# Kernel tuning notes

Hardware: AMD Instinct MI355X
Metric: run time of the kernel (lower is better)

## Reference

```python
import jax, jax.numpy as jnp
from jax import lax
import numpy as np

B, DIM, H, W = 1, 1024, 24, 24
HEADS, GROUPS = 8, 4
TOPK_FRAC = 0.8
EPS = 1e-12


def setup_inputs() -> dict:
    key = jax.random.key(0)
    ks = jax.random.split(key, 5)
    t = GROUPS
    x = jax.random.normal(ks[0], (B, DIM, H, W), dtype=jnp.float32)
    # Conv3d(t, 3t, 1x1x1, bias=False): weight [3t, t]
    w_qkv = jax.random.normal(ks[1], (3 * t, t), dtype=jnp.float32) * 0.3
    # depthwise Conv3d(3t, 3t, (1,3,3), groups=3t): weight [3t, 3, 3]
    w_dw = jax.random.normal(ks[2], (3 * t, 3, 3), dtype=jnp.float32) * 0.2
    # temperature [1, heads, 1, 1]
    temperature = jnp.ones((1, HEADS, 1, 1), dtype=jnp.float32)
    # project_out Conv2d(dim, dim, 1): weight [dim, dim]
    w_proj = jax.random.normal(ks[3], (DIM, DIM), dtype=jnp.float32) * 0.02
    return {"x": x, "temperature": temperature, "w_qkv": w_qkv, "w_dw": w_dw, "w_proj": w_proj}


def _to_heads(u, b, t, cs, h, w):
    # [b, t, cs, h, w] -> [b, heads, ch, (h w t)]  (t fastest in flattened axis)
    ch = cs // HEADS
    u = u.reshape(b, t, HEADS, ch, h, w)
    u = u.transpose(0, 2, 3, 4, 5, 1)  # b, head, ch, h, w, t
    return u.reshape(b, HEADS, ch, h * w * t)


def reference(x, temperature, w_qkv, w_dw, w_proj):
    b, c, h, w = x.shape
    t = GROUPS
    cs = c // t
    xg = x.reshape(b, t, cs, h, w)
    # pointwise conv3d across group dim: [b, 3t, cs, h, w]
    qkv = jnp.einsum("btchw,st->bschw", xg, w_qkv)
    # depthwise (1,3,3) conv: fold cs into batch, 2D depthwise over (h, w)
    y = qkv.transpose(0, 2, 1, 3, 4).reshape(b * cs, 3 * t, h, w)
    kern = w_dw[:, None, :, :]  # [3t, 1, 3, 3]
    y = lax.conv_general_dilated(
        y, kern, window_strides=(1, 1), padding="SAME",
        dimension_numbers=("NCHW", "OIHW", "NCHW"), feature_group_count=3 * t)
    qkv = y.reshape(b, cs, 3 * t, h, w).transpose(0, 2, 1, 3, 4)
    q, k, v = qkv[:, :t], qkv[:, t:2 * t], qkv[:, 2 * t:]
    q = _to_heads(q, b, t, cs, h, w)
    k = _to_heads(k, b, t, cs, h, w)
    v = _to_heads(v, b, t, cs, h, w)
    # L2-normalize over token axis (dim=-1), torch eps semantics
    q = q / jnp.maximum(jnp.linalg.norm(q, axis=-1, keepdims=True), EPS)
    k = k / jnp.maximum(jnp.linalg.norm(k, axis=-1, keepdims=True), EPS)
    N = q.shape[-1]
    K = int(N * TOPK_FRAC)
    attn = jnp.einsum("bhcn,bhcm->bhnm", q, k) * temperature  # [b, heads, N, N]
    vals, idx = lax.top_k(attn, K)
    # scatter top-k values into a -inf matrix == where(mask>0, attn, -inf)
    bi = jnp.arange(b)[:, None, None, None]
    hi = jnp.arange(HEADS)[None, :, None, None]
    ni = jnp.arange(N)[None, None, :, None]
    masked = jnp.full_like(attn, -jnp.inf).at[bi, hi, ni, idx].set(vals)
    p = jax.nn.softmax(masked, axis=-1)
    out = jnp.einsum("bhnm,bhcm->bhcn", p, v)  # [b, heads, ch, N]
    ch = cs // HEADS
    out = out.reshape(b, HEADS, ch, h, w, t).transpose(0, 5, 1, 2, 3, 4).reshape(b, c, h, w)
    out = jnp.einsum("bchw,oc->bohw", out, w_proj)
    return x + out
```

## Files before the change

### kernel.cpp

```cpp
#include <hip/hip_runtime.h>
#include <math.h>

typedef unsigned int u32;
typedef unsigned long long u64;
typedef unsigned short u16;
typedef __attribute__((ext_vector_type(8))) short bf16x8;
typedef __attribute__((ext_vector_type(4))) float f32x4;

#define NHEADS 8
#define HH 24
#define WW 24
#define HW 576
#define CS 256
#define CHD 32
#define NN 2304
#define NGROUPS 4
#define TOPK 1843
#define DIM 1024
#define EPSN 1e-12f

__device__ __forceinline__ u32 fkey(float f) {
    u32 u = __float_as_uint(f);
    return u ^ ((u >> 31) ? 0xFFFFFFFFu : 0x80000000u);
}
__device__ __forceinline__ float fkey_inv(u32 k) {
    return __uint_as_float((k & 0x80000000u) ? (k ^ 0x80000000u) : ~k);
}
__device__ __forceinline__ u16 f2bf(float f) {
    u32 u = __float_as_uint(f);
    return (u16)((u + 0x7FFFu + ((u >> 16) & 1u)) >> 16);
}
__device__ __forceinline__ u32 shiftOf(u32 rg) {
    return (rg > 255u) ? (u32)(24 - __clz(rg)) : 0u;
}

__global__ __launch_bounds__(256) void qkv_conv_kernel(
    const float* __restrict__ x, const float* __restrict__ w_qkv,
    const float* __restrict__ w_dw,
    float* __restrict__ qb, float* __restrict__ kb, u16* __restrict__ vb16)
{
    __shared__ float xp[NGROUPS][26][26];
    __shared__ float wq[48];
    __shared__ float wd[108];
    int c = blockIdx.x;
    int tid = threadIdx.x;

    for (int i = tid; i < NGROUPS * 26 * 26; i += 256) ((float*)xp)[i] = 0.f;
    if (tid < 48) wq[tid] = w_qkv[tid];
    if (tid < 108) wd[tid] = w_dw[tid];
    __syncthreads();
    for (int i = tid; i < NGROUPS * HW; i += 256) {
        int t = i / HW, p = i % HW;
        int hh = p / WW, ww = p % WW;
        xp[t][hh + 1][ww + 1] = x[(size_t)(t * CS + c) * HW + p];
    }
    __syncthreads();

    int hd = c >> 5, ch = c & 31;
    for (int p = tid; p < HW; p += 256) {
        int hh = p / WW, ww = p % WW;
        float res[12];
        #pragma unroll
        for (int s = 0; s < 12; ++s) {
            float acc = 0.f;
            #pragma unroll
            for (int t = 0; t < NGROUPS; ++t) {
                float cv = 0.f;
                #pragma unroll
                for (int dh = 0; dh < 3; ++dh)
                    #pragma unroll
                    for (int dw = 0; dw < 3; ++dw)
                        cv += xp[t][hh + dh][ww + dw] * wd[s * 9 + dh * 3 + dw];
                acc += wq[s * 4 + t] * cv;
            }
            res[s] = acc;
        }
        #pragma unroll
        for (int tt = 0; tt < 4; ++tt) {
            int n = p * 4 + tt;
            size_t off = ((size_t)hd * CHD + ch) * NN + n;
            qb[off] = res[tt];
            kb[off] = res[4 + tt];
            vb16[off] = f2bf(res[8 + tt]);
        }
    }
}

__global__ __launch_bounds__(256) void norm_scale_kernel(
    const float* __restrict__ qb, const float* __restrict__ kb,
    float* __restrict__ scales)
{
    __shared__ float redf[5];
    int b = blockIdx.x;
    const float* rowp = ((b < 256) ? qb : kb) + (size_t)(b & 255) * NN;
    int tid = threadIdx.x;
    float ss = 0.f;
    for (int i = tid; i < NN; i += 256) { float v = rowp[i]; ss += v * v; }
    for (int off = 32; off > 0; off >>= 1) ss += __shfl_down(ss, off);
    int wid = tid >> 6, lane = tid & 63;
    if (lane == 0) redf[wid] = ss;
    __syncthreads();
    if (tid == 0)
        scales[b] = 1.f / fmaxf(sqrtf(redf[0] + redf[1] + redf[2] + redf[3]), EPSN);
}

__global__ __launch_bounds__(256) void transpose_cast_kernel(
    const float* __restrict__ qb, const float* __restrict__ kb,
    const float* __restrict__ scales,
    u16* __restrict__ Qt, u16* __restrict__ Kt)
{
    __shared__ float tile[32][33];
    int ntile = blockIdx.x;
    int h = blockIdx.y;
    int which = blockIdx.z;
    const float* src = which ? kb : qb;
    const float* scl = scales + which * 256;
    u16* dst = which ? Kt : Qt;
    int tid = threadIdx.x;
    int n0 = ntile * 32;
    #pragma unroll
    for (int cc = 0; cc < 32; cc += 8) {
        int c = cc + (tid >> 5);
        tile[c][tid & 31] = src[(size_t)(h * CHD + c) * NN + n0 + (tid & 31)]
                            * scl[h * CHD + c];
    }
    __syncthreads();
    int cgrp = tid & 7, nrow = tid >> 3;
    #pragma unroll
    for (int c0 = 0; c0 < 32; c0 += 16) {
        int c = c0 + cgrp * 2;
        u16 v0 = f2bf(tile[c][nrow]);
        u16 v1 = f2bf(tile[c + 1][nrow]);
        ushort2 v; v.x = v0; v.y = v1;
        *(ushort2*)(dst + ((size_t)h * NN + n0 + nrow) * CHD + c) = v;
    }
}

__global__ __launch_bounds__(256) void cast_wproj_kernel(
    const float* __restrict__ wp, u16* __restrict__ wpb)
{
    int i = blockIdx.x * 256 + threadIdx.x;
    float4 v = ((const float4*)wp)[i];
    ushort4 o;
    o.x = f2bf(v.x); o.y = f2bf(v.y); o.z = f2bf(v.z); o.w = f2bf(v.w);
    ((ushort4*)wpb)[i] = o;
}

__global__ __launch_bounds__(512, 2) void attn_fused3_kernel(
    const u16* __restrict__ Qt, const u16* __restrict__ Kt,
    const u16* __restrict__ Vb, const float* __restrict__ temp,
    u16* __restrict__ aoutT)
{
    __shared__ u32 hist[16][257];
    __shared__ u32 candK[16][64];
    __shared__ u32 candM[16][64];
    __shared__ u16 Pst[8][16][40];
    __shared__ u32 kminA[16], maxkA[16], shA[16], kloA[16], khiA[16],
                   remKA[16], stateA[16], TkeyA[16], candCnt[16];
    __shared__ int cutA[16];
    __shared__ float denomF[16];
    __shared__ u32 flagS;

    int tid = threadIdx.x;
    int lane = tid & 63;
    int w = tid >> 6;
    int q = lane >> 4;
    int cI = lane & 15;
    int h = blockIdx.x / 144;
    int n0 = (blockIdx.x % 144) * 16;

    for (int i = tid; i < 16 * 257; i += 512) ((u32*)hist)[i] = 0u;
    if (tid < 16) {
        kminA[tid] = 0xFFFFFFFFu; maxkA[tid] = 0u; candCnt[tid] = 0u;
        denomF[tid] = 0.f; stateA[tid] = 0u; cutA[tid] = NN - 1;
        remKA[tid] = TOPK; TkeyA[tid] = 0u;
    }
    __syncthreads();

    const u16* Qth = Qt + (size_t)h * NN * CHD;
    const u16* Kth = Kt + (size_t)h * NN * CHD;
    const u16* Vbh = Vb + (size_t)h * CHD * NN;
    float ts = temp[h];

    bf16x8 afrag = *(const bf16x8*)(Qth + (size_t)(n0 + cI) * CHD + q * 8);
    int mW = w * 288;
    const f32x4 zz = {0.f, 0.f, 0.f, 0.f};

    {
        u32 lmin[4], lmax[4];
        #pragma unroll
        for (int r = 0; r < 4; ++r) { lmin[r] = 0xFFFFFFFFu; lmax[r] = 0u; }
        #pragma unroll 2
        for (int t = 0; t < 18; ++t) {
            bf16x8 bfrag = *(const bf16x8*)(Kth + (size_t)(mW + t * 16 + cI) * CHD + q * 8);
            f32x4 a = __builtin_amdgcn_mfma_f32_16x16x32_bf16(afrag, bfrag, zz, 0, 0, 0);
            #pragma unroll
            for (int r = 0; r < 4; ++r) {
                u32 k = fkey(a[r] * ts);
                lmin[r] = min(lmin[r], k); lmax[r] = max(lmax[r], k);
            }
        }
        #pragma unroll
        for (int r = 0; r < 4; ++r) {
            #pragma unroll
            for (int mk = 1; mk < 16; mk <<= 1) {
                lmin[r] = min(lmin[r], (u32)__shfl_xor((int)lmin[r], mk));
                lmax[r] = max(lmax[r], (u32)__shfl_xor((int)lmax[r], mk));
            }
            if (cI == 0) {
                atomicMin(&kminA[4 * q + r], lmin[r]);
                atomicMax(&maxkA[4 * q + r], lmax[r]);
            }
        }
    }
    __syncthreads();
    if (tid < 16) shA[tid] = shiftOf(maxkA[tid] - kminA[tid]);
    __syncthreads();

    {
        u32 km[4], sh[4];
        #pragma unroll
        for (int r = 0; r < 4; ++r) { km[r] = kminA[4 * q + r]; sh[r] = shA[4 * q + r]; }
        #pragma unroll 2
        for (int t = 0; t < 18; ++t) {
            bf16x8 bfrag = *(const bf16x8*)(Kth + (size_t)(mW + t * 16 + cI) * CHD + q * 8);
            f32x4 a = __builtin_amdgcn_mfma_f32_16x16x32_bf16(afrag, bfrag, zz, 0, 0, 0);
            #pragma unroll
            for (int r = 0; r < 4; ++r) {
                u32 k = fkey(a[r] * ts);
                atomicAdd(&hist[4 * q + r][(k - km[r]) >> sh[r]], 1u);
            }
        }
    }
    __syncthreads();

    #pragma unroll
    for (int rr = 0; rr < 2; ++rr) {
        int r = 2 * w + rr;
        u32 c0 = hist[r][lane * 4 + 0];
        u32 c1 = hist[r][lane * 4 + 1];
        u32 c2 = hist[r][lane * 4 + 2];
        u32 c3 = hist[r][lane * 4 + 3];
        u32 s3 = c3, s2 = c2 + s3, s1 = c1 + s2, s0 = c0 + s1;
        u32 suf = s0;
        #pragma unroll
        for (int off = 1; off < 64; off <<= 1) {
            u32 t2 = (u32)__shfl_down((int)suf, off);
            if (lane + off < 64) suf += t2;
        }
        u32 above_lane = suf - s0;
        u32 sArr[4] = {s0, s1, s2, s3};
        u32 cArr[4] = {c0, c1, c2, c3};
        u32 km = kminA[r], sh = shA[r];
        #pragma unroll
        for (int i = 0; i < 4; ++i) {
            u32 S = above_lane + sArr[i];
            u32 cb = cArr[i];
            if (S >= TOPK && S - cb < TOPK) {
                u32 b = lane * 4 + i;
                u32 klo = km + (b << sh);
                u64 khiL = (u64)km + ((u64)(b + 1) << sh) - 1ull;
                u32 khi = (khiL > 0xFFFFFFFFull) ? 0xFFFFFFFFu : (u32)khiL;
                kloA[r] = klo; khiA[r] = khi;
                remKA[r] = TOPK - (S - cb);
                if (cb <= 64u) stateA[r] = 1u;
                else if (klo == khi) { stateA[r] = 3u; TkeyA[r] = klo; }
                else stateA[r] = 0u;
            }
        }
    }
    __syncthreads();

    for (int round = 0; round < 4; ++round) {
        if (tid == 0) {
            u32 any = 0;
            for (int r = 0; r < 16; ++r) any |= (stateA[r] == 0u) ? 1u : 0u;
            flagS = any;
        }
        __syncthreads();
        if (!flagS) break;
        if (tid < 257) {
            for (int r = 0; r < 16; ++r)
                if (stateA[r] == 0u) hist[r][tid] = 0u;
        }
        __syncthreads();
        {
            u32 st2[4], kl2[4], sh2[4], kh2[4];
            #pragma unroll
            for (int r = 0; r < 4; ++r) {
                int row = 4 * q + r;
                st2[r] = stateA[row]; kl2[r] = kloA[row]; kh2[r] = khiA[row];
                sh2[r] = shiftOf(kh2[r] - kl2[r]);
            }
            #pragma unroll 2
            for (int t = 0; t < 18; ++t) {
                bf16x8 bfrag = *(const bf16x8*)(Kth + (size_t)(mW + t * 16 + cI) * CHD + q * 8);
                f32x4 a = __builtin_amdgcn_mfma_f32_16x16x32_bf16(afrag, bfrag, zz, 0, 0, 0);
                #pragma unroll
                for (int r = 0; r < 4; ++r) {
                    if (st2[r] == 0u) {
                        u32 k = fkey(a[r] * ts);
                        if (k >= kl2[r] && k <= kh2[r])
                            atomicAdd(&hist[4 * q + r][(k - kl2[r]) >> sh2[r]], 1u);
                    }
                }
            }
        }
        __syncthreads();
        #pragma unroll
        for (int rr = 0; rr < 2; ++rr) {
            int r = 2 * w + rr;
            if (stateA[r] != 0u) continue;
            u32 klo = kloA[r], khi = khiA[r];
            u32 sh = shiftOf(khi - klo);
            u32 c0 = hist[r][lane * 4 + 0];
            u32 c1 = hist[r][lane * 4 + 1];
            u32 c2 = hist[r][lane * 4 + 2];
            u32 c3 = hist[r][lane * 4 + 3];
            u32 s3 = c3, s2 = c2 + s3, s1 = c1 + s2, s0 = c0 + s1;
            u32 suf = s0;
            #pragma unroll
            for (int off = 1; off < 64; off <<= 1) {
                u32 t2 = (u32)__shfl_down((int)suf, off);
                if (lane + off < 64) suf += t2;
            }
            u32 above_lane = suf - s0;
            u32 remK = remKA[r];
            u32 sArr[4] = {s0, s1, s2, s3};
            u32 cArr[4] = {c0, c1, c2, c3};
            #pragma unroll
            for (int i = 0; i < 4; ++i) {
                u32 S = above_lane + sArr[i];
                u32 cb = cArr[i];
                if (S >= remK && S - cb < remK) {
                    u32 b = lane * 4 + i;
                    u32 nlo = klo + (b << sh);
                    u64 nhiL = (u64)klo + ((u64)(b + 1) << sh) - 1ull;
                    u32 nhi = (nhiL > (u64)khi) ? khi : (u32)nhiL;
                    kloA[r] = nlo; khiA[r] = nhi;
                    remKA[r] = remK - (S - cb);
                    if (cb <= 64u) stateA[r] = 1u;
                    else if (nlo == nhi) { stateA[r] = 3u; TkeyA[r] = nlo; }
                    else stateA[r] = 0u;
                }
            }
        }
        __syncthreads();
    }
    if (tid < 16 && stateA[tid] == 0u) {
        TkeyA[tid] = kloA[tid]; stateA[tid] = 3u;
    }
    __syncthreads();

    {
        u32 st[4], kl[4], kh[4];
        #pragma unroll
        for (int r = 0; r < 4; ++r) {
            int row = 4 * q + r;
            st[r] = stateA[row]; kl[r] = kloA[row]; kh[r] = khiA[row];
        }
        #pragma unroll 2
        for (int t = 0; t < 18; ++t) {
            bf16x8 bfrag = *(const bf16x8*)(Kth + (size_t)(mW + t * 16 + cI) * CHD + q * 8);
            f32x4 a = __builtin_amdgcn_mfma_f32_16x16x32_bf16(afrag, bfrag, zz, 0, 0, 0);
            int m = mW + t * 16 + cI;
            #pragma unroll
            for (int r = 0; r < 4; ++r) {
                if (st[r] == 1u) {
                    u32 k = fkey(a[r] * ts);
                    if (k >= kl[r] && k <= kh[r]) {
                        int row = 4 * q + r;
                        u32 pos = atomicAdd(&candCnt[row], 1u);
                        if (pos < 64u) { candK[row][pos] = k; candM[row][pos] = (u32)m; }
                    }
                }
            }
        }
    }
    __syncthreads();

    #pragma unroll
    for (int rr = 0; rr < 2; ++rr) {
        int r = 2 * w + rr;
        if (stateA[r] == 1u) {
            u32 cnt = min(candCnt[r], 64u);
            u32 remK = remKA[r];
            u32 myk = 0u, mym = 0u;
            if (lane < (int)cnt) { myk = candK[r][lane]; mym = candM[r][lane]; }
            u32 gtr = 0;
            for (u32 i = 0; i < cnt; ++i) {
                u32 ki = candK[r][i], mi = candM[r][i];
                gtr += (ki > myk || (ki == myk && mi < mym)) ? 1u : 0u;
            }
            if (lane < (int)cnt && gtr == remK - 1u) {
                TkeyA[r] = myk; cutA[r] = (int)mym;
            }
        }
    }
    __syncthreads();

    {
        float maxf[4], ls[4];
        u32 Tr[4]; int cutr[4];
        #pragma unroll
        for (int r = 0; r < 4; ++r) {
            int row = 4 * q + r;
            maxf[r] = fkey_inv(maxkA[row]);
            Tr[r] = TkeyA[row];
            cutr[r] = cutA[row];
            ls[r] = 0.f;
        }
        f32x4 acc0 = {0.f, 0.f, 0.f, 0.f};
        f32x4 acc1 = {0.f, 0.f, 0.f, 0.f};
        for (int j = 0; j < 9; ++j) {
            int mb = mW + j * 32;
            bf16x8 b0 = *(const bf16x8*)(Kth + (size_t)(mb + cI) * CHD + q * 8);
            bf16x8 b1 = *(const bf16x8*)(Kth + (size_t)(mb + 16 + cI) * CHD + q * 8);
            f32x4 a0 = __builtin_amdgcn_mfma_f32_16x16x32_bf16(afrag, b0, zz, 0, 0, 0);
            f32x4 a1 = __builtin_amdgcn_mfma_f32_16x16x32_bf16(afrag, b1, zz, 0, 0, 0);
            #pragma unroll
            for (int r = 0; r < 4; ++r) {
                {
                    float s = a0[r] * ts;
                    u32 k = fkey(s);
                    int m = mb + cI;
                    bool inc = (k > Tr[r]) || (k == Tr[r] && m <= cutr[r]);
                    float p = inc ? __expf(s - maxf[r]) : 0.f;
                    ls[r] += p;
                    Pst[w][4 * q + r][cI] = f2bf(p);
                }
                {
                    float s = a1[r] * ts;
                    u32 k = fkey(s);
                    int m = mb + 16 + cI;
                    bool inc = (k > Tr[r]) || (k == Tr[r] && m <= cutr[r]);
                    float p = inc ? __expf(s - maxf[r]) : 0.f;
                    ls[r] += p;
                    Pst[w][4 * q + r][16 + cI] = f2bf(p);
                }
            }
            bf16x8 pf = *(const bf16x8*)&Pst[w][cI][q * 8];
            bf16x8 v0 = *(const bf16x8*)(Vbh + (size_t)cI * NN + mb + q * 8);
            bf16x8 v1 = *(const bf16x8*)(Vbh + (size_t)(16 + cI) * NN + mb + q * 8);
            acc0 = __builtin_amdgcn_mfma_f32_16x16x32_bf16(v0, pf, acc0, 0, 0, 0);
            acc1 = __builtin_amdgcn_mfma_f32_16x16x32_bf16(v1, pf, acc1, 0, 0, 0);
        }
        #pragma unroll
        for (int r = 0; r < 4; ++r) {
            #pragma unroll
            for (int mk = 1; mk < 16; mk <<= 1)
                ls[r] += __shfl_xor(ls[r], mk);
            if (cI == 0) atomicAdd(&denomF[4 * q + r], ls[r]);
        }
        __syncthreads();
        float* red = (float*)hist;
        #pragma unroll
        for (int r = 0; r < 4; ++r) {
            red[((size_t)w * 32 + (4 * q + r)) * 16 + cI] = acc0[r];
            red[((size_t)w * 32 + 16 + (4 * q + r)) * 16 + cI] = acc1[r];
        }
    }
    __syncthreads();

    {
        const float* red = (const float*)hist;
        int c = tid >> 4, n = tid & 15;
        float s = 0.f;
        #pragma unroll
        for (int w2 = 0; w2 < 8; ++w2) s += red[((size_t)w2 * 32 + c) * 16 + n];
        s /= denomF[n];
        int ng = n0 + n;
        int t = ng & 3, p = ng >> 2;
        aoutT[(size_t)p * DIM + t * CS + h * CHD + c] = f2bf(s);
    }
}

__global__ __launch_bounds__(256) void proj_mfma_kernel(
    const u16* __restrict__ aoutT, const u16* __restrict__ wpb,
    const float* __restrict__ x, float* __restrict__ out)
{
    int tid = threadIdx.x, lane = tid & 63, w = tid >> 6;
    int q = lane >> 4, cI = lane & 15;
    int p0 = blockIdx.x * 16;
    int o0 = blockIdx.y * 64 + w * 16;
    f32x4 acc = {0.f, 0.f, 0.f, 0.f};
    const u16* arow = wpb + (size_t)(o0 + cI) * DIM + q * 8;
    const u16* brow = aoutT + (size_t)(p0 + cI) * DIM + q * 8;
    #pragma unroll 8
    for (int k = 0; k < DIM; k += 32) {
        bf16x8 af = *(const bf16x8*)(arow + k);
        bf16x8 bf = *(const bf16x8*)(brow + k);
        acc = __builtin_amdgcn_mfma_f32_16x16x32_bf16(af, bf, acc, 0, 0, 0);
    }
    #pragma unroll
    for (int r = 0; r < 4; ++r) {
        int o = o0 + 4 * q + r, p = p0 + cI;
        out[(size_t)o * HW + p] = x[(size_t)o * HW + p] + acc[r];
    }
}

extern "C" void kernel_launch(void* const* d_in, const int* in_sizes, int n_in,
                              void* d_out, int out_size, void* d_ws, size_t ws_size,
                              hipStream_t stream)
{
    const float* x     = (const float*)d_in[0];
    const float* temp  = (const float*)d_in[1];
    const float* w_qkv = (const float*)d_in[2];
    const float* w_dw  = (const float*)d_in[3];
    const float* wproj = (const float*)d_in[4];
    float* out = (float*)d_out;

    const size_t T = (size_t)NHEADS * CHD * NN;
    char* ws = (char*)d_ws;
    float* qb    = (float*)(ws);
    float* kb    = (float*)(ws + 4 * T);
    u16*   Qt    = (u16*)(ws + 8 * T);
    u16*   Kt    = (u16*)(ws + 10 * T);
    u16*   Vb    = (u16*)(ws + 12 * T);
    u16*   aoutT = (u16*)(ws + 14 * T);
    u16*   wpb   = (u16*)(ws + 16 * T);
    float* scales= (float*)(ws + 16 * T + (size_t)DIM * DIM * 2);

    qkv_conv_kernel<<<256, 256, 0, stream>>>(x, w_qkv, w_dw, qb, kb, Vb);
    norm_scale_kernel<<<512, 256, 0, stream>>>(qb, kb, scales);
    transpose_cast_kernel<<<dim3(72, 8, 2), 256, 0, stream>>>(qb, kb, scales, Qt, Kt);
    cast_wproj_kernel<<<DIM * DIM / 4 / 256, 256, 0, stream>>>(wproj, wpb);
    attn_fused3_kernel<<<NHEADS * 144, 512, 0, stream>>>(Qt, Kt, Vb, temp, aoutT);
    proj_mfma_kernel<<<dim3(36, 16), 256, 0, stream>>>(aoutT, wpb, x, out);
}
```

Before: 154.0 us.

## Fuse top-k candidate collection into softmax pass and resolve boundary afterward

Removes the separate QK^T recompute pass that gathered candidates in the threshold bin. Candidates are now collected during the softmax/PV pass, with their exp values stored in shared memory. Ties are resolved afterward and the accepted boundary terms are added to the denominator and output through scalar V gathers. Separately, the qkv conv kernel moves to 512 threads per block. The change saves one full pass of MFMA and K loads per tile, at the cost of extra atomics and a serial candidate loop in the epilogue.

```diff
diff --git a/kernel.cpp b/kernel.cpp
--- a/kernel.cpp
+++ b/kernel.cpp
@@ -30,11 +30,14 @@
     u32 u = __float_as_uint(f);
     return (u16)((u + 0x7FFFu + ((u >> 16) & 1u)) >> 16);
 }
+__device__ __forceinline__ float bf2f(u16 b) {
+    return __uint_as_float(((u32)b) << 16);
+}
 __device__ __forceinline__ u32 shiftOf(u32 rg) {
     return (rg > 255u) ? (u32)(24 - __clz(rg)) : 0u;
 }
 
-__global__ __launch_bounds__(256) void qkv_conv_kernel(
+__global__ __launch_bounds__(512) void qkv_conv_kernel(
     const float* __restrict__ x, const float* __restrict__ w_qkv,
     const float* __restrict__ w_dw,
     float* __restrict__ qb, float* __restrict__ kb, u16* __restrict__ vb16)
@@ -45,11 +48,11 @@
     int c = blockIdx.x;
     int tid = threadIdx.x;
 
-    for (int i = tid; i < NGROUPS * 26 * 26; i += 256) ((float*)xp)[i] = 0.f;
+    for (int i = tid; i < NGROUPS * 26 * 26; i += 512) ((float*)xp)[i] = 0.f;
     if (tid < 48) wq[tid] = w_qkv[tid];
     if (tid < 108) wd[tid] = w_dw[tid];
     __syncthreads();
-    for (int i = tid; i < NGROUPS * HW; i += 256) {
+    for (int i = tid; i < NGROUPS * HW; i += 512) {
         int t = i / HW, p = i % HW;
         int hh = p / WW, ww = p % WW;
         xp[t][hh + 1][ww + 1] = x[(size_t)(t * CS + c) * HW + p];
@@ -57,7 +60,7 @@
     __syncthreads();
 
     int hd = c >> 5, ch = c & 31;
-    for (int p = tid; p < HW; p += 256) {
+    for (int p = tid; p < HW; p += 512) {
         int hh = p / WW, ww = p % WW;
         float res[12];
         #pragma unroll
@@ -146,7 +149,7 @@
     ((ushort4*)wpb)[i] = o;
 }
 
-__global__ __launch_bounds__(512, 2) void attn_fused3_kernel(
+__global__ __launch_bounds__(512, 2) void attn_fused4_kernel(
     const u16* __restrict__ Qt, const u16* __restrict__ Kt,
     const u16* __restrict__ Vb, const float* __restrict__ temp,
     u16* __restrict__ aoutT)
@@ -154,10 +157,10 @@
     __shared__ u32 hist[16][257];
     __shared__ u32 candK[16][64];
     __shared__ u32 candM[16][64];
+    __shared__ float candP[16][64];
     __shared__ u16 Pst[8][16][40];
     __shared__ u32 kminA[16], maxkA[16], shA[16], kloA[16], khiA[16],
-                   remKA[16], stateA[16], TkeyA[16], candCnt[16];
-    __shared__ int cutA[16];
+                   remKA[16], stateA[16], candCnt[16];
     __shared__ float denomF[16];
     __shared__ u32 flagS;
 
@@ -172,8 +175,7 @@
     for (int i = tid; i < 16 * 257; i += 512) ((u32*)hist)[i] = 0u;
     if (tid < 16) {
         kminA[tid] = 0xFFFFFFFFu; maxkA[tid] = 0u; candCnt[tid] = 0u;
-        denomF[tid] = 0.f; stateA[tid] = 0u; cutA[tid] = NN - 1;
-        remKA[tid] = TOPK; TkeyA[tid] = 0u;
+        denomF[tid] = 0.f; stateA[tid] = 0u; remKA[tid] = TOPK;
     }
     __syncthreads();
 
@@ -264,7 +266,7 @@
                 kloA[r] = klo; khiA[r] = khi;
                 remKA[r] = TOPK - (S - cb);
                 if (cb <= 64u) stateA[r] = 1u;
-                else if (klo == khi) { stateA[r] = 3u; TkeyA[r] = klo; }
+                else if (klo == khi) stateA[r] = 3u;
                 else stateA[r] = 0u;
             }
         }
@@ -340,7 +342,7 @@
                     kloA[r] = nlo; khiA[r] = nhi;
                     remKA[r] = remK - (S - cb);
                     if (cb <= 64u) stateA[r] = 1u;
-                    else if (nlo == nhi) { stateA[r] = 3u; TkeyA[r] = nlo; }
+                    else if (nlo == nhi) stateA[r] = 3u;
                     else stateA[r] = 0u;
                 }
             }
@@ -348,70 +350,22 @@
         __syncthreads();
     }
     if (tid < 16 && stateA[tid] == 0u) {
-        TkeyA[tid] = kloA[tid]; stateA[tid] = 3u;
-    }
-    __syncthreads();
-
-    {
-        u32 st[4], kl[4], kh[4];
-        #pragma unroll
-        for (int r = 0; r < 4; ++r) {
-            int row = 4 * q + r;
-            st[r] = stateA[row]; kl[r] = kloA[row]; kh[r] = khiA[row];
-        }
-        #pragma unroll 2
-        for (int t = 0; t < 18; ++t) {
-            bf16x8 bfrag = *(const bf16x8*)(Kth + (size_t)(mW + t * 16 + cI) * CHD + q * 8);
-            f32x4 a = __builtin_amdgcn_mfma_f32_16x16x32_bf16(afrag, bfrag, zz, 0, 0, 0);
-            int m = mW + t * 16 + cI;
-            #pragma unroll
-            for (int r = 0; r < 4; ++r) {
-                if (st[r] == 1u) {
-                    u32 k = fkey(a[r] * ts);
-                    if (k >= kl[r] && k <= kh[r]) {
-                        int row = 4 * q + r;
-                        u32 pos = atomicAdd(&candCnt[row], 1u);
-                        if (pos < 64u) { candK[row][pos] = k; candM[row][pos] = (u32)m; }
-                    }
-                }
-            }
-        }
-    }
-    __syncthreads();
-
-    #pragma unroll
-    for (int rr = 0; rr < 2; ++rr) {
-        int r = 2 * w + rr;
-        if (stateA[r] == 1u) {
-            u32 cnt = min(candCnt[r], 64u);
-            u32 remK = remKA[r];
-            u32 myk = 0u, mym = 0u;
-            if (lane < (int)cnt) { myk = candK[r][lane]; mym = candM[r][lane]; }
-            u32 gtr = 0;
-            for (u32 i = 0; i < cnt; ++i) {
-                u32 ki = candK[r][i], mi = candM[r][i];
-                gtr += (ki > myk || (ki == myk && mi < mym)) ? 1u : 0u;
-            }
-            if (lane < (int)cnt && gtr == remK - 1u) {
-                TkeyA[r] = myk; cutA[r] = (int)mym;
-            }
-        }
-    }
-    __syncthreads();
-
+        khiA[tid] = kloA[tid]; stateA[tid] = 3u;
+    }
+    __syncthreads();
+
+    f32x4 acc0 = zz, acc1 = zz;
     {
         float maxf[4], ls[4];
-        u32 Tr[4]; int cutr[4];
+        u32 klo3[4], khi3[4];
         #pragma unroll
         for (int r = 0; r < 4; ++r) {
             int row = 4 * q + r;
             maxf[r] = fkey_inv(maxkA[row]);
-            Tr[r] = TkeyA[row];
-            cutr[r] = cutA[row];
+            klo3[r] = kloA[row];
+            khi3[r] = khiA[row];
             ls[r] = 0.f;
         }
-        f32x4 acc0 = {0.f, 0.f, 0.f, 0.f};
-        f32x4 acc1 = {0.f, 0.f, 0.f, 0.f};
         for (int j = 0; j < 9; ++j) {
             int mb = mW + j * 32;
             bf16x8 b0 = *(const bf16x8*)(Kth + (size_t)(mb + cI) * CHD + q * 8);
@@ -423,18 +377,32 @@
                 {
                     float s = a0[r] * ts;
                     u32 k = fkey(s);
-                    int m = mb + cI;
-                    bool inc = (k > Tr[r]) || (k == Tr[r] && m <= cutr[r]);
-                    float p = inc ? __expf(s - maxf[r]) : 0.f;
+                    float e = __expf(s - maxf[r]);
+                    float p = (k > khi3[r]) ? e : 0.f;
+                    if (k >= klo3[r] && k <= khi3[r]) {
+                        int row = 4 * q + r;
+                        u32 pos = atomicAdd(&candCnt[row], 1u);
+                        if (pos < 64u) {
+                            candK[row][pos] = k; candM[row][pos] = (u32)(mb + cI);
+                            candP[row][pos] = e;
+                        }
+                    }
                     ls[r] += p;
                     Pst[w][4 * q + r][cI] = f2bf(p);
                 }
                 {
                     float s = a1[r] * ts;
                     u32 k = fkey(s);
-                    int m = mb + 16 + cI;
-                    bool inc = (k > Tr[r]) || (k == Tr[r] && m <= cutr[r]);
-                    float p = inc ? __expf(s - maxf[r]) : 0.f;
+                    float e = __expf(s - maxf[r]);
+                    float p = (k > khi3[r]) ? e : 0.f;
+                    if (k >= klo3[r] && k <= khi3[r]) {
+                        int row = 4 * q + r;
+                        u32 pos = atomicAdd(&candCnt[row], 1u);
+                        if (pos < 64u) {
+                            candK[row][pos] = k; candM[row][pos] = (u32)(mb + 16 + cI);
+                            candP[row][pos] = e;
+                        }
+                    }
                     ls[r] += p;
                     Pst[w][4 * q + r][16 + cI] = f2bf(p);
                 }
@@ -452,7 +420,34 @@
                 ls[r] += __shfl_xor(ls[r], mk);
             if (cI == 0) atomicAdd(&denomF[4 * q + r], ls[r]);
         }
-        __syncthreads();
+    }
+    __syncthreads();
+
+    #pragma unroll
+    for (int rr = 0; rr < 2; ++rr) {
+        int r = 2 * w + rr;
+        u32 cnt = min(candCnt[r], 64u);
+        u32 remK = remKA[r];
+        u32 myk = 0u, mym = 0xFFFFFFFFu;
+        float myp = 0.f;
+        if (lane < (int)cnt) {
+            myk = candK[r][lane]; mym = candM[r][lane]; myp = candP[r][lane];
+        }
+        u32 gtr = 0;
+        for (u32 i = 0; i < cnt; ++i) {
+            u32 ki = candK[r][i], mi = candM[r][i];
+            gtr += (ki > myk || (ki == myk && mi < mym)) ? 1u : 0u;
+        }
+        bool accept = (lane < (int)cnt) && (gtr < remK);
+        float pacc = accept ? myp : 0.f;
+        candP[r][lane] = pacc;
+        float psum = pacc;
+        #pragma unroll
+        for (int off = 32; off > 0; off >>= 1) psum += __shfl_down(psum, off);
+        if (lane == 0) denomF[r] += psum;
+    }
+
+    {
         float* red = (float*)hist;
         #pragma unroll
         for (int r = 0; r < 4; ++r) {
@@ -468,10 +463,16 @@
         float s = 0.f;
         #pragma unroll
         for (int w2 = 0; w2 < 8; ++w2) s += red[((size_t)w2 * 32 + c) * 16 + n];
+        u32 cnt = min(candCnt[n], 64u);
+        const u16* Vc = Vbh + (size_t)c * NN;
+        for (u32 i = 0; i < cnt; ++i) {
+            float p = candP[n][i];
+            if (p != 0.f) s += p * bf2f(Vc[candM[n][i]]);
+        }
         s /= denomF[n];
         int ng = n0 + n;
-        int t = ng & 3, p = ng >> 2;
-        aoutT[(size_t)p * DIM + t * CS + h * CHD + c] = f2bf(s);
+        int t = ng & 3, pp = ng >> 2;
+        aoutT[(size_t)pp * DIM + t * CS + h * CHD + c] = f2bf(s);
     }
 }
 
@@ -521,10 +522,10 @@
     u16*   wpb   = (u16*)(ws + 16 * T);
     float* scales= (float*)(ws + 16 * T + (size_t)DIM * DIM * 2);
 
-    qkv_conv_kernel<<<256, 256, 0, stream>>>(x, w_qkv, w_dw, qb, kb, Vb);
+    qkv_conv_kernel<<<256, 512, 0, stream>>>(x, w_qkv, w_dw, qb, kb, Vb);
     norm_scale_kernel<<<512, 256, 0, stream>>>(qb, kb, scales);
     transpose_cast_kernel<<<dim3(72, 8, 2), 256, 0, stream>>>(qb, kb, scales, Qt, Kt);
     cast_wproj_kernel<<<DIM * DIM / 4 / 256, 256, 0, stream>>>(wproj, wpb);
-    attn_fused3_kernel<<<NHEADS * 144, 512, 0, stream>>>(Qt, Kt, Vb, temp, aoutT);
+    attn_fused4_kernel<<<NHEADS * 144, 512, 0, stream>>>(Qt, Kt, Vb, temp, aoutT);
     proj_mfma_kernel<<<dim3(36, 16), 256, 0, stream>>>(aoutT, wpb, x, out);
 }
```

Measured after the change: 156.3 us. No clear change (+1.5%).
